# Optimization experiments

Measured on AMD Instinct MI355X. Metric: run time of the kernel, lower is better.

Reference implementation:

```python
import jax, jax.numpy as jnp
import numpy as np
from jax import lax

B, A, K = 16, 200000, 300          # batch, anchors, NMS candidate cap
THR_CONF, THR_NMS = 0.5, 0.3
VAR0, VAR1 = 0.1, 0.2              # RetinaFace decode variances


def setup_inputs() -> dict:
    key = jax.random.key(0)
    k1, k2, k3, k4, k5 = jax.random.split(key, 5)
    p_loc = jax.random.normal(k1, (B, A, 4), jnp.float32) * 0.5
    p_conf = jax.random.normal(k2, (B, A, 1), jnp.float32) - 2.0
    p_landms = jax.random.normal(k3, (B, A, 10), jnp.float32) * 0.5
    cxy = jax.random.uniform(k4, (A, 2), jnp.float32)
    wh = 0.01 + 0.09 * jax.random.uniform(k5, (A, 2), jnp.float32)
    anchors = jnp.concatenate([cxy, wh], axis=-1)   # [A,4] cx,cy,w,h in [0,1]
    return {"p_loc": p_loc, "p_conf": p_conf, "p_landms": p_landms, "anchors": anchors}


def _decode_boxes_ltrb(anchors, loc):
    # fix_bbox: cxy = a_cxy + loc[:2]*0.1*a_wh ; wh = a_wh * exp(loc[2:]*0.2)
    a = anchors[None]                              # [1,A,4]
    cxy = a[..., :2] + loc[..., :2] * VAR0 * a[..., 2:]
    wh = a[..., 2:] * jnp.exp(loc[..., 2:] * VAR1)
    half = 0.5 * wh
    return jnp.concatenate([cxy - half, cxy + half], axis=-1)  # xywh2ltrb -> [B,A,4]


def _decode_keypoints(anchors, landms):
    # fix_keypoints: 5 points, each a_cxy + d*0.1*a_wh (computed in original fwd; unused in outputs)
    a = anchors[None]
    d = landms.reshape(landms.shape[0], landms.shape[1], 5, 2)
    kp = a[..., None, :2] + d * VAR0 * a[..., None, 2:]
    return kp.reshape(landms.shape)


def _iou_matrix(b):  # b [K,4] ltrb -> [K,K]
    lt = jnp.maximum(b[:, None, :2], b[None, :, :2])
    rb = jnp.minimum(b[:, None, 2:], b[None, :, 2:])
    wh = jnp.clip(rb - lt, 0.0)
    inter = wh[..., 0] * wh[..., 1]
    area = jnp.clip(b[:, 2] - b[:, 0], 0.0) * jnp.clip(b[:, 3] - b[:, 1], 0.0)
    union = area[:, None] + area[None, :] - inter
    return inter / jnp.maximum(union, 1e-9)


def _nms_keep(boxes, valid):
    # boxes already sorted by descending score; greedy NMS over K candidates
    iou = _iou_matrix(boxes)
    idx = jnp.arange(K)
    def body(i, keep):
        sup = keep[i] & (iou[i] > THR_NMS) & (idx > i)
        return keep & ~sup
    return lax.fori_loop(0, K, body, valid)


def reference(p_loc, p_conf, p_landms, anchors):
    scores = jax.nn.sigmoid(p_conf[..., 0])                     # [B,A]
    boxes_ltrb = _decode_boxes_ltrb(anchors, p_loc)             # [B,A,4]
    _ = _decode_keypoints(anchors, p_landms)                    # faithful dead compute

    mask = scores >= THR_CONF
    masked_scores = jnp.where(mask, scores, 0.0)
    top_scores, top_idx = lax.top_k(masked_scores, K)           # [B,K] sorted desc
    top_boxes = jnp.take_along_axis(boxes_ltrb, top_idx[..., None], axis=1)  # [B,K,4]
    valid = top_scores >= THR_CONF

    keep = jax.vmap(_nms_keep)(top_boxes, valid)                # [B,K] bool
    keep_f = keep.astype(top_scores.dtype)

    ids_batch2 = jnp.where(keep, jnp.broadcast_to(jnp.arange(B)[:, None], (B, K)), -1).reshape(-1)
    p_boxes_ltrb2 = (top_boxes * keep_f[..., None]).reshape(-1, 4)
    p_scores2 = (top_scores * keep_f).reshape(-1)
    p_labels2 = keep_f.reshape(-1)   # original labels are all ones; zero on padded slots
    return ids_batch2, p_boxes_ltrb2, p_labels2, p_scores2, keep.reshape(-1)
```

## Files before the change

kernel.cpp:

```cpp
#include <hip/hip_runtime.h>
#include <cstdint>

typedef unsigned int u32;
typedef unsigned long long u64;

#define B 16
#define A 200000
#define K 300
#define CAP 8192

__global__ __launch_bounds__(256) void scan_kernel(const float* __restrict__ p_conf,
                                                   u64* __restrict__ cand,
                                                   u32* __restrict__ cnt) {
    __shared__ u64 lbuf[1024];
    __shared__ u32 lcnt;
    __shared__ u32 lbase;
    const int b = blockIdx.y;
    const int f4 = blockIdx.x * 256 + threadIdx.x;

    if (threadIdx.x == 0) lcnt = 0;
    __syncthreads();

    if (f4 < A / 4) {
        const float4 c4 = ((const float4*)(p_conf + (size_t)b * A))[f4];
        const float xs[4] = {c4.x, c4.y, c4.z, c4.w};
        #pragma unroll
        for (int e = 0; e < 4; ++e) {
            const float x = xs[e];
            if (x >= -0.001f) {
                float s = 1.0f / (1.0f + expf(-x));
                if (s >= 0.5f) {
                    u32 sb  = __float_as_uint(s);
                    u32 idx = (u32)(f4 * 4 + e);
                    u64 key = ((u64)sb << 32) | (u64)(0xFFFFFFFFu - idx);
                    u32 p = atomicAdd(&lcnt, 1u);
                    lbuf[p] = key;
                }
            }
        }
    }
    __syncthreads();
    if (threadIdx.x == 0 && lcnt > 0) lbase = atomicAdd(&cnt[b], lcnt);
    __syncthreads();
    const u32 total = lcnt;
    for (u32 t = threadIdx.x; t < total; t += 256) {
        u32 g = lbase + t;
        if (g < CAP) cand[(size_t)b * CAP + g] = lbuf[t];
    }
}

__global__ __launch_bounds__(512) void select_nms_kernel(
    const float* __restrict__ p_loc,
    const float* __restrict__ anchors,
    const u64* __restrict__ cand,
    const u32* __restrict__ cnt,
    float* __restrict__ out) {

    __shared__ u32 hist[512];
    __shared__ u32 sfx[512];
    __shared__ u32 wsum[8];
    __shared__ u64 buf[1024];
    __shared__ u64 skey[K];
    __shared__ float sl[K], st_[K], sr[K], sb_[K], sar[K];
    __shared__ u64 mask[K][5];
    __shared__ u64 keepw[5];
    __shared__ u32 sh_cut, sh_m;

    const int b    = blockIdx.x;
    const int tid  = threadIdx.x;
    const int lane = tid & 63;
    const int wv   = tid >> 6;
    const u32 c    = min(cnt[b], (u32)CAP);
    const u32 need = min((u32)K, c);
    const u64* mycand = cand + (size_t)b * CAP;

    hist[tid] = 0;
    {   u64* mf = &mask[0][0];
        for (int i = tid; i < K * 5; i += 512) mf[i] = 0ull; }
    if (tid == 0) { sh_m = 0; sh_cut = 0; }
    __syncthreads();

    for (u32 i = tid; i < c; i += 512) {
        u32 sb  = (u32)(mycand[i] >> 32);
        u32 bin = min((sb - 0x3F000000u) >> 14, 511u);
        atomicAdd(&hist[bin], 1u);
    }
    __syncthreads();

    u32 s = hist[tid];
    #pragma unroll
    for (int off = 1; off < 64; off <<= 1) {
        u32 t = __shfl_down(s, off, 64);
        if (lane + off < 64) s += t;
    }
    if (lane == 0) wsum[wv] = s;
    __syncthreads();
    u32 tail = 0;
    #pragma unroll
    for (int w = 0; w < 8; ++w) if (w > wv) tail += wsum[w];
    sfx[tid] = s + tail;
    __syncthreads();

    if (need > 0) {
        if (sfx[tid] >= need && (tid == 511 || sfx[tid + 1] < need)) sh_cut = (u32)tid;
    }
    __syncthreads();

    const u32 cut = sh_cut;
    for (u32 i = tid; i < c; i += 512) {
        u64 kk  = mycand[i];
        u32 sb  = (u32)(kk >> 32);
        u32 bin = min((sb - 0x3F000000u) >> 14, 511u);
        if (bin >= cut) {
            u32 p = atomicAdd(&sh_m, 1u);
            if (p < 1024) buf[p] = kk;
        }
    }
    __syncthreads();
    const u32 M = min(sh_m, 1024u);

    for (u32 t = tid; t < M; t += 512) {
        const u64 mykey = buf[t];
        u32 r = 0;
        #pragma unroll 4
        for (u32 j = 0; j < M; ++j) r += (buf[j] > mykey) ? 1u : 0u;
        if (r < (u32)K) skey[r] = mykey;
    }
    __syncthreads();

    const u32 S = need;
    float dl = 0.f, dt = 0.f, dr = 0.f, db = 0.f, dsc = 0.f;
    if (tid < K) {
        float ar = 0.f;
        if ((u32)tid < S) {
            u64 kk = skey[tid];
            dsc = __uint_as_float((u32)(kk >> 32));
            u32 aidx = 0xFFFFFFFFu - (u32)(kk & 0xFFFFFFFFull);
            const float4 loc = ((const float4*)p_loc)[(size_t)b * A + aidx];
            const float4 an  = ((const float4*)anchors)[aidx];
            float cx = an.x + loc.x * 0.1f * an.z;
            float cy = an.y + loc.y * 0.1f * an.w;
            float w  = an.z * expf(loc.z * 0.2f);
            float h  = an.w * expf(loc.w * 0.2f);
            dl = cx - 0.5f * w; dt = cy - 0.5f * h;
            dr = cx + 0.5f * w; db = cy + 0.5f * h;
            ar = fmaxf(dr - dl, 0.0f) * fmaxf(db - dt, 0.0f);
        }
        sl[tid] = dl; st_[tid] = dt; sr[tid] = dr; sb_[tid] = db; sar[tid] = ar;
    }
    __syncthreads();

    {
        int r, j0, jstep; bool active;
        if (tid < K) { r = tid;     j0 = r + 1; jstep = (r < 212) ? 2 : 1; active = ((u32)r < S); }
        else         { r = tid - K; j0 = r + 2; jstep = 2;                 active = ((u32)r < S); }
        if (active) {
            const float li = sl[r], ti = st_[r], ri = sr[r], bi = sb_[r], ai = sar[r];
            u64 acc = 0; int wcur = j0 >> 6;
            for (int j = j0; j < (int)S; j += jstep) {
                const int w = j >> 6;
                if (w != wcur) {
                    if (acc) atomicOr(&mask[r][wcur], acc);
                    acc = 0; wcur = w;
                }
                float lt0 = fmaxf(li, sl[j]);
                float lt1 = fmaxf(ti, st_[j]);
                float rb0 = fminf(ri, sr[j]);
                float rb1 = fminf(bi, sb_[j]);
                float iw = fmaxf(rb0 - lt0, 0.0f);
                float ih = fmaxf(rb1 - lt1, 0.0f);
                float inter = iw * ih;
                float uni = ai + sar[j] - inter;
                float iou = inter / fmaxf(uni, 1e-9f);
                if (iou > 0.3f) acc |= (1ull << (j & 63));
            }
            if (acc) atomicOr(&mask[r][wcur], acc);
        }
    }
    __syncthreads();

    if (wv == 0) {
        u64 kw = 0;
        if (lane < 5) {
            int rem = (int)S - lane * 64;
            kw = rem <= 0 ? 0ull : (rem >= 64 ? ~0ull : ((1ull << rem) - 1ull));
        }
        for (int i = 0; i < (int)S; ++i) {
            u64 srcw = __shfl(kw, i >> 6);
            if ((srcw >> (i & 63)) & 1ull) {
                u64 row = mask[i][lane < 5 ? lane : 0];
                if (lane < 5) kw &= ~row;
            }
        }
        if (lane < 5) keepw[lane] = kw;
    }
    __syncthreads();

    if (tid < K) {
        const int g = b * K + tid;
        const bool kept = (keepw[tid >> 6] >> (tid & 63)) & 1ull;
        out[g] = kept ? (float)b : -1.0f;
        float* obox = out + B * K + (size_t)g * 4;
        obox[0] = kept ? dl : 0.0f;
        obox[1] = kept ? dt : 0.0f;
        obox[2] = kept ? dr : 0.0f;
        obox[3] = kept ? db : 0.0f;
        out[B * K * 5 + g] = kept ? 1.0f : 0.0f;
        out[B * K * 6 + g] = kept ? dsc : 0.0f;
        out[B * K * 7 + g] = kept ? 1.0f : 0.0f;
    }
}

extern "C" void kernel_launch(void* const* d_in, const int* in_sizes, int n_in,
                              void* d_out, int out_size, void* d_ws, size_t ws_size,
                              hipStream_t stream) {
    const float* p_loc   = (const float*)d_in[0];
    const float* p_conf  = (const float*)d_in[1];
    const float* anchors = (const float*)d_in[3];
    float* out = (float*)d_out;

    u64* cand = (u64*)d_ws;
    u32* cnt  = (u32*)((char*)d_ws + (size_t)B * CAP * 8);

    hipMemsetAsync(cnt, 0, B * sizeof(u32), stream);

    dim3 gridA((A / 4 + 255) / 256, B);
    scan_kernel<<<gridA, 256, 0, stream>>>(p_conf, cand, cnt);
    select_nms_kernel<<<B, 512, 0, stream>>>(p_loc, anchors, cand, cnt, out);
}
```

Before: 289.3 us.

## Use per-block candidate regions and parallel fixed-point NMS resolution

The scan kernel now writes each block's candidates to a fixed per-block region with its own count, which removes the global atomic counter and the memset launch. The select kernel walks those regions per wave. The serial single-wave greedy NMS loop is replaced by a block-wide fixed-point iteration: each round ORs the suppression rows of currently kept boxes via shuffles and atomics, and it stops once the keep set no longer changes. This can take many rounds, each with several barriers, and it relies on the fixed point matching greedy NMS.

```diff
diff --git a/kernel.cpp b/kernel.cpp
--- a/kernel.cpp
+++ b/kernel.cpp
@@ -7,16 +7,16 @@
 #define B 16
 #define A 200000
 #define K 300
-#define CAP 8192
+#define NREG 196
 
 __global__ __launch_bounds__(256) void scan_kernel(const float* __restrict__ p_conf,
                                                    u64* __restrict__ cand,
                                                    u32* __restrict__ cnt) {
     __shared__ u64 lbuf[1024];
     __shared__ u32 lcnt;
-    __shared__ u32 lbase;
-    const int b = blockIdx.y;
-    const int f4 = blockIdx.x * 256 + threadIdx.x;
+    const int b  = blockIdx.y;
+    const int bx = blockIdx.x;
+    const int f4 = bx * 256 + threadIdx.x;
 
     if (threadIdx.x == 0) lcnt = 0;
     __syncthreads();
@@ -40,13 +40,10 @@
         }
     }
     __syncthreads();
-    if (threadIdx.x == 0 && lcnt > 0) lbase = atomicAdd(&cnt[b], lcnt);
-    __syncthreads();
     const u32 total = lcnt;
-    for (u32 t = threadIdx.x; t < total; t += 256) {
-        u32 g = lbase + t;
-        if (g < CAP) cand[(size_t)b * CAP + g] = lbuf[t];
-    }
+    u64* dst = cand + ((size_t)(b * NREG + bx) << 10);
+    for (u32 t = threadIdx.x; t < total; t += 256) dst[t] = lbuf[t];
+    if (threadIdx.x == 0) cnt[b * NREG + bx] = total;
 }
 
 __global__ __launch_bounds__(512) void select_nms_kernel(
@@ -56,6 +53,7 @@
     const u32* __restrict__ cnt,
     float* __restrict__ out) {
 
+    __shared__ u32 scnt[NREG];
     __shared__ u32 hist[512];
     __shared__ u32 sfx[512];
     __shared__ u32 wsum[8];
@@ -63,27 +61,30 @@
     __shared__ u64 skey[K];
     __shared__ float sl[K], st_[K], sr[K], sb_[K], sar[K];
     __shared__ u64 mask[K][5];
-    __shared__ u64 keepw[5];
+    __shared__ u64 validw[5], kcur[5], sup[5];
+    __shared__ int s_changed;
     __shared__ u32 sh_cut, sh_m;
 
     const int b    = blockIdx.x;
     const int tid  = threadIdx.x;
     const int lane = tid & 63;
     const int wv   = tid >> 6;
-    const u32 c    = min(cnt[b], (u32)CAP);
-    const u32 need = min((u32)K, c);
-    const u64* mycand = cand + (size_t)b * CAP;
 
     hist[tid] = 0;
     {   u64* mf = &mask[0][0];
         for (int i = tid; i < K * 5; i += 512) mf[i] = 0ull; }
+    for (int i = tid; i < NREG; i += 512) scnt[i] = cnt[b * NREG + i];
     if (tid == 0) { sh_m = 0; sh_cut = 0; }
     __syncthreads();
 
-    for (u32 i = tid; i < c; i += 512) {
-        u32 sb  = (u32)(mycand[i] >> 32);
-        u32 bin = min((sb - 0x3F000000u) >> 14, 511u);
-        atomicAdd(&hist[bin], 1u);
+    for (int r = wv; r < NREG; r += 8) {
+        const u32 kr = scnt[r];
+        const u64* p = cand + ((size_t)(b * NREG + r) << 10);
+        for (u32 i = lane; i < kr; i += 64) {
+            u32 sb  = (u32)(p[i] >> 32);
+            u32 bin = min((sb - 0x3F000000u) >> 14, 511u);
+            atomicAdd(&hist[bin], 1u);
+        }
     }
     __syncthreads();
 
@@ -101,19 +102,25 @@
     sfx[tid] = s + tail;
     __syncthreads();
 
+    const u32 need = min((u32)K, sfx[0]);
     if (need > 0) {
         if (sfx[tid] >= need && (tid == 511 || sfx[tid + 1] < need)) sh_cut = (u32)tid;
     }
     __syncthreads();
 
     const u32 cut = sh_cut;
-    for (u32 i = tid; i < c; i += 512) {
-        u64 kk  = mycand[i];
-        u32 sb  = (u32)(kk >> 32);
-        u32 bin = min((sb - 0x3F000000u) >> 14, 511u);
-        if (bin >= cut) {
-            u32 p = atomicAdd(&sh_m, 1u);
-            if (p < 1024) buf[p] = kk;
+    if (need > 0) {
+        for (int r = wv; r < NREG; r += 8) {
+            const u32 kr = scnt[r];
+            const u64* p = cand + ((size_t)(b * NREG + r) << 10);
+            for (u32 i = lane; i < kr; i += 64) {
+                u64 kk  = p[i];
+                u32 bin = min(((u32)(kk >> 32) - 0x3F000000u) >> 14, 511u);
+                if (bin >= cut) {
+                    u32 q = atomicAdd(&sh_m, 1u);
+                    if (q < 1024) buf[q] = kk;
+                }
+            }
         }
     }
     __syncthreads();
@@ -177,28 +184,56 @@
             if (acc) atomicOr(&mask[r][wcur], acc);
         }
     }
-    __syncthreads();
-
-    if (wv == 0) {
-        u64 kw = 0;
-        if (lane < 5) {
-            int rem = (int)S - lane * 64;
-            kw = rem <= 0 ? 0ull : (rem >= 64 ? ~0ull : ((1ull << rem) - 1ull));
-        }
-        for (int i = 0; i < (int)S; ++i) {
-            u64 srcw = __shfl(kw, i >> 6);
-            if ((srcw >> (i & 63)) & 1ull) {
-                u64 row = mask[i][lane < 5 ? lane : 0];
-                if (lane < 5) kw &= ~row;
-            }
-        }
-        if (lane < 5) keepw[lane] = kw;
-    }
-    __syncthreads();
+
+    u64 m0 = 0, m1 = 0, m2 = 0, m3 = 0, m4 = 0;
+    __syncthreads();
+    if ((u32)tid < S) {
+        m0 = mask[tid][0]; m1 = mask[tid][1]; m2 = mask[tid][2];
+        m3 = mask[tid][3]; m4 = mask[tid][4];
+    }
+    if (tid < 5) {
+        int rem = (int)S - tid * 64;
+        u64 v = rem <= 0 ? 0ull : (rem >= 64 ? ~0ull : ((1ull << rem) - 1ull));
+        validw[tid] = v; kcur[tid] = v;
+    }
+    __syncthreads();
+
+    for (u32 it = 0; it <= S; ++it) {
+        if (tid < 5) sup[tid] = 0;
+        if (tid == 0) s_changed = 0;
+        __syncthreads();
+        u64 c0 = 0, c1 = 0, c2 = 0, c3 = 0, c4 = 0;
+        if ((u32)tid < S) {
+            u64 kw = kcur[tid >> 6];
+            if ((kw >> (tid & 63)) & 1ull) { c0 = m0; c1 = m1; c2 = m2; c3 = m3; c4 = m4; }
+        }
+        #pragma unroll
+        for (int off = 1; off < 64; off <<= 1) {
+            c0 |= __shfl_xor(c0, off, 64);
+            c1 |= __shfl_xor(c1, off, 64);
+            c2 |= __shfl_xor(c2, off, 64);
+            c3 |= __shfl_xor(c3, off, 64);
+            c4 |= __shfl_xor(c4, off, 64);
+        }
+        if (lane == 0) {
+            if (c0) atomicOr(&sup[0], c0);
+            if (c1) atomicOr(&sup[1], c1);
+            if (c2) atomicOr(&sup[2], c2);
+            if (c3) atomicOr(&sup[3], c3);
+            if (c4) atomicOr(&sup[4], c4);
+        }
+        __syncthreads();
+        if (tid < 5) {
+            u64 nk = validw[tid] & ~sup[tid];
+            if (nk != kcur[tid]) { s_changed = 1; kcur[tid] = nk; }
+        }
+        __syncthreads();
+        if (!s_changed) break;
+    }
 
     if (tid < K) {
         const int g = b * K + tid;
-        const bool kept = (keepw[tid >> 6] >> (tid & 63)) & 1ull;
+        const bool kept = (kcur[tid >> 6] >> (tid & 63)) & 1ull;
         out[g] = kept ? (float)b : -1.0f;
         float* obox = out + B * K + (size_t)g * 4;
         obox[0] = kept ? dl : 0.0f;
@@ -220,11 +255,9 @@
     float* out = (float*)d_out;
 
     u64* cand = (u64*)d_ws;
-    u32* cnt  = (u32*)((char*)d_ws + (size_t)B * CAP * 8);
-
-    hipMemsetAsync(cnt, 0, B * sizeof(u32), stream);
-
-    dim3 gridA((A / 4 + 255) / 256, B);
+    u32* cnt  = (u32*)((char*)d_ws + (size_t)B * NREG * 1024 * 8);
+
+    dim3 gridA(NREG, B);
     scan_kernel<<<gridA, 256, 0, stream>>>(p_conf, cand, cnt);
     select_nms_kernel<<<B, 512, 0, stream>>>(p_loc, anchors, cand, cnt, out);
 }
```

Measured after the change: 247.7 us. -14.4%, faster.
